# Performance work log

Hardware: AMD Instinct MI355X
Metric: run time of the kernel (lower is better)

## Reference

```python
import jax, jax.numpy as jnp
import numpy as np

WINDOWS = ((0, 4), (2, 6), (4, 8))
N_CLASSES = 64
EPS = 1e-12  # F.normalize eps


def setup_inputs() -> dict:
    key = jax.random.key(0)
    k1, k2 = jax.random.split(key)
    S, Q, T, D = 256, 4096, 8, 1024
    support_features = jax.random.normal(k1, (S, T, D), dtype=jnp.float32)
    target_features = jax.random.normal(k2, (Q, T, D), dtype=jnp.float32)
    support_labels = jnp.arange(S, dtype=jnp.int32) % N_CLASSES  # 4 shots per class, sorted-unique order
    logit_scale = jnp.array(0.0, dtype=jnp.float32)
    fusion_logits = jnp.zeros((3,), dtype=jnp.float32)
    return {
        'support_features': support_features,
        'target_features': target_features,
        'support_labels': support_labels,
        'logit_scale': logit_scale,
        'fusion_logits': fusion_logits,
    }


def _l2norm(x):
    n = jnp.sqrt(jnp.sum(x * x, axis=-1, keepdims=True))
    return x / jnp.maximum(n, EPS)


def _pairwise_dist(query_seq, support_seq):
    # query_seq: [Q, Tq, D], support_seq: [K, Ts, D] -> 1 - cosine sim [Q, K, Tq, Ts]
    sim = jnp.einsum('qtd,ksd->qkts', _l2norm(query_seq), _l2norm(support_seq))
    return 1.0 - sim


def _bi_mhm(dists):
    # dists: [Q, K, Tq, Ts]
    return dists.min(axis=3).sum(axis=2) + dists.min(axis=2).sum(axis=2)


def _segments(features):
    # features: [N, T, D] -> [N, n_windows, D] (mean over each window)
    return jnp.stack([features[:, s:e, :].mean(axis=1) for s, e in WINDOWS], axis=1)


def _prototypes(features, labels):
    # scatter-mean over class labels; features: [S, ...], labels: [S]
    sums = jax.ops.segment_sum(features, labels, num_segments=N_CLASSES)
    counts = jax.ops.segment_sum(jnp.ones((features.shape[0],), features.dtype), labels,
                                 num_segments=N_CLASSES)
    return sums / counts[:, None, None]


def reference(support_features, target_features, support_labels, logit_scale, fusion_logits):
    # global (frame-level) bidirectional min-sum chamfer distance to class prototypes
    support_proto = _prototypes(support_features, support_labels)          # [K, T, D]
    global_dist = _bi_mhm(_pairwise_dist(target_features, support_proto))  # [Q, K]

    # segment-level distances
    support_segments = _segments(support_features)                          # [S, 3, D]
    target_segments = _segments(target_features)                            # [Q, 3, D]
    support_seg_proto = _prototypes(support_segments, support_labels)       # [K, 3, D]
    seg_dist = _pairwise_dist(target_segments, support_seg_proto)           # [Q, K, 3, 3]
    seg_q2s = seg_dist.min(axis=3).sum(axis=2)
    seg_s2q = seg_dist.min(axis=2).sum(axis=2)

    fusion = jax.nn.softmax(fusion_logits)
    fused = (fusion[0] * global_dist + fusion[1] * seg_s2q + fusion[2] * seg_q2s)
    fused = fused * jnp.exp(logit_scale)
    return (-fused, -global_dist, -seg_s2q, -seg_q2s)
```

## Files before the change

### kernel.cpp

```cpp
#include <hip/hip_runtime.h>
#include <stdint.h>

typedef unsigned short u16;
typedef short short8 __attribute__((ext_vector_type(8)));
typedef float floatx4 __attribute__((ext_vector_type(4)));

#define KDIM 1024
#define QN   4096
#define KCLS 64
#define QK   (QN * KCLS)

#define DPP_XOR1 0xB1
#define DPP_XOR2 0x4E
#define DPP_HMIR 0x141
#define SWZ_XOR6  0x181F
#define SWZ_XOR16 0x401F

template <int CTRL>
__device__ __forceinline__ float dppf(float x) {
  int r = __builtin_amdgcn_mov_dpp(__builtin_bit_cast(int, x), CTRL, 0xF, 0xF, true);
  return __builtin_bit_cast(float, r);
}
template <int OFF>
__device__ __forceinline__ float swzf(float x) {
  int r = __builtin_amdgcn_ds_swizzle(__builtin_bit_cast(int, x), OFF);
  return __builtin_bit_cast(float, r);
}
__device__ __forceinline__ float max8(float x) {
  x = fmaxf(x, dppf<DPP_XOR1>(x));
  x = fmaxf(x, dppf<DPP_XOR2>(x));
  x = fmaxf(x, dppf<DPP_HMIR>(x));
  return x;
}
__device__ __forceinline__ float sum8(float x) {
  x += dppf<DPP_XOR1>(x);
  x += dppf<DPP_XOR2>(x);
  x += dppf<DPP_HMIR>(x);
  return x;
}


__device__ __forceinline__ u16 f2bf(float x) {
  union { float f; uint32_t u; } un; un.f = x;
  uint32_t u = un.u;
  u += 0x7FFFu + ((u >> 16) & 1u);
  return (u16)(u >> 16);
}

struct alignas(16) F4 { float x, y, z, w; };
struct alignas(8)  U16x4 { u16 a, b, c, d; };

__device__ __forceinline__ float dot4(const F4& a, const F4& b) {
  return a.x*b.x + a.y*b.y + a.z*b.z + a.w*b.w;
}

__device__ __forceinline__ void reduce11(float (&ss)[11], float (&tot)[11],
                                         float (*sb)[12], int lane, int wave) {
  #pragma unroll
  for (int v = 0; v < 11; ++v) {
    float x = ss[v];
    #pragma unroll
    for (int m = 1; m < 64; m <<= 1) x += __shfl_xor(x, m);
    ss[v] = x;
  }
  if (lane == 0) {
    #pragma unroll
    for (int v = 0; v < 11; ++v) sb[wave][v] = ss[v];
  }
  __syncthreads();
  #pragma unroll
  for (int v = 0; v < 11; ++v)
    tot[v] = sb[0][v] + sb[1][v] + sb[2][v] + sb[3][v];
}

__device__ __forceinline__ float inv_norm(float ss) {
  return 1.0f / fmaxf(sqrtf(ss), 1e-12f);
}

__global__ __launch_bounds__(256) void prep_all(const float* __restrict__ T,
                                                const float* __restrict__ S,
                                                u16* __restrict__ Ag,
                                                u16* __restrict__ Bg,
                                                float* __restrict__ invnT,
                                                float* __restrict__ invnTw,
                                                float* __restrict__ invnS,
                                                float* __restrict__ invnSw) {
  __shared__ float sb[4][12];
  const int b = blockIdx.x, tid = threadIdx.x;
  const int lane = tid & 63, wave = tid >> 6;

  if (b < QN) {
    const int q = b;
    F4 x[8];
    #pragma unroll
    for (int t = 0; t < 8; ++t)
      x[t] = *(const F4*)(T + (size_t)(q*8 + t)*1024 + tid*4);

    float ss[11], tot[11];
    #pragma unroll
    for (int t = 0; t < 8; ++t) ss[t] = dot4(x[t], x[t]);
    #pragma unroll
    for (int w = 0; w < 3; ++w) {
      F4 y;
      y.x = (x[2*w].x + x[2*w+1].x + x[2*w+2].x + x[2*w+3].x) * 0.25f;
      y.y = (x[2*w].y + x[2*w+1].y + x[2*w+2].y + x[2*w+3].y) * 0.25f;
      y.z = (x[2*w].z + x[2*w+1].z + x[2*w+2].z + x[2*w+3].z) * 0.25f;
      y.w = (x[2*w].w + x[2*w+1].w + x[2*w+2].w + x[2*w+3].w) * 0.25f;
      ss[8+w] = dot4(y, y);
    }
    reduce11(ss, tot, sb, lane, wave);

    #pragma unroll
    for (int t = 0; t < 8; ++t) {
      U16x4 o; o.a = f2bf(x[t].x); o.b = f2bf(x[t].y);
      o.c = f2bf(x[t].z); o.d = f2bf(x[t].w);
      *(U16x4*)(Ag + (size_t)(q*8 + t)*1024 + tid*4) = o;
    }
    if (tid < 8)       invnT [q*8 + tid]     = inv_norm(tot[tid]);
    else if (tid < 11) invnTw[q*4 + tid - 8] = inv_norm(tot[tid]);
  } else {
    const int k = b - QN;
    F4 p[8];
    #pragma unroll
    for (int t = 0; t < 8; ++t) { p[t].x = 0.f; p[t].y = 0.f; p[t].z = 0.f; p[t].w = 0.f; }
    #pragma unroll
    for (int s = 0; s < 4; ++s)
      #pragma unroll
      for (int t = 0; t < 8; ++t) {
        const F4 v = *(const F4*)(S + (size_t)(((s*64 + k)*8 + t))*1024 + tid*4);
        p[t].x += v.x; p[t].y += v.y; p[t].z += v.z; p[t].w += v.w;
      }
    float ss[11], tot[11];
    #pragma unroll
    for (int t = 0; t < 8; ++t) ss[t] = dot4(p[t], p[t]) * 0.0625f;
    #pragma unroll
    for (int w = 0; w < 3; ++w) {
      F4 y;
      y.x = (p[2*w].x + p[2*w+1].x + p[2*w+2].x + p[2*w+3].x) * 0.0625f;
      y.y = (p[2*w].y + p[2*w+1].y + p[2*w+2].y + p[2*w+3].y) * 0.0625f;
      y.z = (p[2*w].z + p[2*w+1].z + p[2*w+2].z + p[2*w+3].z) * 0.0625f;
      y.w = (p[2*w].w + p[2*w+1].w + p[2*w+2].w + p[2*w+3].w) * 0.0625f;
      ss[8+w] = dot4(y, y);
    }
    reduce11(ss, tot, sb, lane, wave);

    #pragma unroll
    for (int t = 0; t < 8; ++t) {
      U16x4 o; o.a = f2bf(p[t].x*0.25f); o.b = f2bf(p[t].y*0.25f);
      o.c = f2bf(p[t].z*0.25f); o.d = f2bf(p[t].w*0.25f);
      *(U16x4*)(Bg + (size_t)(k*8 + t)*1024 + tid*4) = o;
    }
    if (tid < 8)       invnS [k*8 + tid]     = inv_norm(tot[tid]);
    else if (tid < 11) invnSw[k*4 + tid - 8] = inv_norm(tot[tid]) * 0.0625f;
  }
}


__device__ __forceinline__ void load_lds16(const u16* g, u16* l) {
  __builtin_amdgcn_global_load_lds((__attribute__((address_space(1))) void*)(g),
                                   (__attribute__((address_space(3))) void*)(l),
                                   16, 0, 0);
}

__global__ __launch_bounds__(1024) void gemm_all(const u16* __restrict__ A,
                                                 const u16* __restrict__ B,
                                                 const float* __restrict__ invnT,
                                                 const float* __restrict__ invnTw,
                                                 const float* __restrict__ invnS,
                                                 const float* __restrict__ invnSw,
                                                 float* __restrict__ outF,
                                                 float* __restrict__ outG,
                                                 float* __restrict__ outS2Q,
                                                 float* __restrict__ outQ2S,
                                                 const float* __restrict__ fl,
                                                 const float* __restrict__ ls) {
  __shared__ __align__(16) u16 At[2][128 * 64];

  const int tid  = threadIdx.x;
  const int lane = tid & 63;
  const int wave = tid >> 6;
  const int wm = wave >> 3;
  const int wn = wave & 7;
  const int rowA0 = blockIdx.x * 128;

  floatx4 acc[4][4] = {};

  const int srow = lane >> 3;
  const int scol = ((lane & 7) ^ srow) * 8;
  const u16* aSrc = A + (size_t)(rowA0 + wave*8 + srow) * KDIM + scol;

  const u16* bBase = B + (size_t)(wn*64 + (lane & 15)) * KDIM + (lane >> 4) * 8;

  int aOff[4];
  #pragma unroll
  for (int i = 0; i < 4; ++i) {
    const int row = wm*64 + i*16 + (lane & 15);
    aOff[i] = row*64 + (((lane >> 4) ^ (row & 7)) * 8);
  }

  load_lds16(aSrc, &At[0][wave * 512]);

  for (int kb_i = 0; kb_i < 16; ++kb_i) {
    const int cur = kb_i & 1;
    __syncthreads();
    if (kb_i < 15)
      load_lds16(aSrc + (kb_i + 1) * 64, &At[cur ^ 1][wave * 512]);

    const u16* Ac = At[cur];
    #pragma unroll
    for (int kk = 0; kk < 2; ++kk) {
      short8 af[4], bf[4];
      #pragma unroll
      for (int i = 0; i < 4; ++i) {
        const int off = aOff[i] ^ (kk * 32);
        af[i] = *(const short8*)&Ac[off];
      }
      #pragma unroll
      for (int j = 0; j < 4; ++j)
        bf[j] = *(const short8*)(bBase + (size_t)j * 16 * KDIM + kb_i * 64 + kk * 32);
      #pragma unroll
      for (int i = 0; i < 4; ++i)
        #pragma unroll
        for (int j = 0; j < 4; ++j)
          acc[i][j] = __builtin_amdgcn_mfma_f32_16x16x32_bf16(af[i], bf[j], acc[i][j], 0, 0, 0);
    }
  }

  const int sIdx = lane & 7;
  const int b3 = (lane >> 3) & 1;
  const int b4 = (lane >> 4) & 1;
  const int b5 = lane >> 5;
  const int qL = blockIdx.x * 16 + wm * 8;
  const int kL = wn * 8;

  float invT[4][4], invTw3[4][3], invS[4], invSw3[4][3];
  #pragma unroll
  for (int i = 0; i < 4; ++i) {
    const int q = qL + i*2 + b5;
    #pragma unroll
    for (int r = 0; r < 4; ++r) invT[i][r] = invnT[q*8 + b4*4 + r];
    #pragma unroll
    for (int w = 0; w < 3; ++w) invTw3[i][w] = invnTw[q*4 + w];
  }
  #pragma unroll
  for (int j = 0; j < 4; ++j) {
    const int k = kL + j*2 + b3;
    invS[j] = invnS[k*8 + sIdx];
    #pragma unroll
    for (int v = 0; v < 3; ++v) invSw3[j][v] = invnSw[k*4 + v];
  }

  const float f0 = fl[0], f1 = fl[1], f2 = fl[2];
  const float mx = fmaxf(f0, fmaxf(f1, f2));
  const float e0 = __expf(f0 - mx), e1 = __expf(f1 - mx), e2 = __expf(f2 - mx);
  const float sc = __expf(ls[0]) / (e0 + e1 + e2);

  const int vA = (sIdx < 4) ? 0 : 2;
  const bool v1ok = (sIdx >= 2) && (sIdx <= 5);

  #pragma unroll
  for (int i = 0; i < 4; ++i) {
    #pragma unroll
    for (int j = 0; j < 4; ++j) {
      const floatx4 c = acc[i][j];

      float sim[4];
      #pragma unroll
      for (int r = 0; r < 4; ++r) sim[r] = c[r] * invT[i][r] * invS[j];
      float rs = 0.f;
      #pragma unroll
      for (int r = 0; r < 4; ++r) rs += max8(sim[r]);
      rs += swzf<SWZ_XOR16>(rs);
      float cm = fmaxf(fmaxf(sim[0], sim[1]), fmaxf(sim[2], sim[3]));
      cm = fmaxf(cm, swzf<SWZ_XOR16>(cm));
      const float cs = sum8(cm);
      const float g = rs + cs - 16.0f;

      float wA[4], wB[4];
      #pragma unroll
      for (int r = 0; r < 4; ++r) {
        const float p2 = c[r] + dppf<DPP_XOR1>(c[r]);
        wA[r] = p2 + dppf<DPP_XOR2>(p2);
        wB[r] = p2 + swzf<SWZ_XOR6>(p2);
      }
      float twA[3], twB[3];
      {
        const float aAll = wA[0] + wA[1] + wA[2] + wA[3];
        const float aOth = swzf<SWZ_XOR16>(aAll);
        twA[0] = b4 ? aOth : aAll;
        twA[2] = b4 ? aAll : aOth;
        const float aH = b4 ? (wA[0] + wA[1]) : (wA[2] + wA[3]);
        twA[1] = aH + swzf<SWZ_XOR16>(aH);
        const float bAll = wB[0] + wB[1] + wB[2] + wB[3];
        const float bOth = swzf<SWZ_XOR16>(bAll);
        twB[0] = b4 ? bOth : bAll;
        twB[2] = b4 ? bAll : bOth;
        const float bH = b4 ? (wB[0] + wB[1]) : (wB[2] + wB[3]);
        twB[1] = bH + swzf<SWZ_XOR16>(bH);
      }
      float pA[3], pB[3];
      #pragma unroll
      for (int w = 0; w < 3; ++w) {
        pA[w] = twA[w] * invTw3[i][w] * invSw3[j][vA];
        pB[w] = twB[w] * invTw3[i][w] * invSw3[j][1];
      }
      float q2s = 0.f;
      #pragma unroll
      for (int w = 0; w < 3; ++w)
        q2s += max8(v1ok ? fmaxf(pA[w], pB[w]) : pA[w]);
      const float mwA = fmaxf(fmaxf(pA[0], pA[1]), pA[2]);
      const float mwB = fmaxf(fmaxf(pB[0], pB[1]), pB[2]);
      float contrib = ((sIdx == 0) | (sIdx == 4)) ? mwA : 0.f;
      if (sIdx == 2) contrib += mwB;
      const float s2q = sum8(contrib);

      if ((lane & 23) == 0) {
        const int q = qL + i*2 + b5;
        const int k = kL + j*2 + b3;
        const size_t idx = (size_t)q * KCLS + k;
        const float o1 = g;
        const float o2 = s2q - 3.0f;
        const float o3 = q2s - 3.0f;
        outG[idx]   = o1;
        outS2Q[idx] = o2;
        outQ2S[idx] = o3;
        outF[idx]   = sc * (e0 * o1 + e1 * o2 + e2 * o3);
      }
    }
  }
}


extern "C" void kernel_launch(void* const* d_in, const int* in_sizes, int n_in,
                              void* d_out, int out_size, void* d_ws, size_t ws_size,
                              hipStream_t stream) {
  (void)in_sizes; (void)n_in; (void)out_size; (void)ws_size;
  const float* S  = (const float*)d_in[0];
  const float* T  = (const float*)d_in[1];
  const float* ls = (const float*)d_in[3];
  const float* fl = (const float*)d_in[4];

  float* outF   = (float*)d_out;
  float* outG   = outF + QK;
  float* outS2Q = outF + 2 * (size_t)QK;
  float* outQ2S = outF + 3 * (size_t)QK;

  u16*   Ag     = (u16*)d_ws;
  u16*   Bg     = Ag + (size_t)32768 * 1024;
  float* invnT  = (float*)(Bg + (size_t)512 * 1024);
  float* invnTw = invnT + 32768;
  float* invnS  = invnTw + 16384;
  float* invnSw = invnS + 512;

  prep_all<<<QN + KCLS, 256, 0, stream>>>(T, S, Ag, Bg, invnT, invnTw, invnS, invnSw);

  gemm_all<<<256, 1024, 0, stream>>>(Ag, Bg, invnT, invnTw, invnS, invnSw,
                                     outF, outG, outS2Q, outQ2S, fl, ls);
}
```

Before: 299.4 us.

## Retile GEMM to 128x128 blocks with A and B staged in LDS

Replaces the 1024-thread block, which covered 128 rows by all 512 B columns and read B fragments straight from global memory, with 256-thread blocks on a 2D grid, each computing a 128x128 tile. Both A and B tiles are loaded into swizzled LDS with direct global-to-LDS loads in 128-wide K chunks. The aim is to reuse B through LDS instead of repeated global reads and to raise the number of blocks for better occupancy. In exchange, A is now read four times, one per grid column, and the K loop loses double buffering, so each chunk's load is separated from compute by barriers.

```diff
diff --git a/kernel.cpp b/kernel.cpp
--- a/kernel.cpp
+++ b/kernel.cpp
@@ -162,62 +162,56 @@
                                    16, 0, 0);
 }
 
-__global__ __launch_bounds__(1024) void gemm_all(const u16* __restrict__ A,
-                                                 const u16* __restrict__ B,
-                                                 const float* __restrict__ invnT,
-                                                 const float* __restrict__ invnTw,
-                                                 const float* __restrict__ invnS,
-                                                 const float* __restrict__ invnSw,
-                                                 float* __restrict__ outF,
-                                                 float* __restrict__ outG,
-                                                 float* __restrict__ outS2Q,
-                                                 float* __restrict__ outQ2S,
-                                                 const float* __restrict__ fl,
-                                                 const float* __restrict__ ls) {
-  __shared__ __align__(16) u16 At[2][128 * 64];
+__global__ __launch_bounds__(256) void gemm_all(const u16* __restrict__ A,
+                                                const u16* __restrict__ B,
+                                                const float* __restrict__ invnT,
+                                                const float* __restrict__ invnTw,
+                                                const float* __restrict__ invnS,
+                                                const float* __restrict__ invnSw,
+                                                float* __restrict__ outF,
+                                                float* __restrict__ outG,
+                                                float* __restrict__ outS2Q,
+                                                float* __restrict__ outQ2S,
+                                                const float* __restrict__ fl,
+                                                const float* __restrict__ ls) {
+  __shared__ __align__(16) u16 At[128 * 128];
+  __shared__ __align__(16) u16 Bt[128 * 128];
 
   const int tid  = threadIdx.x;
   const int lane = tid & 63;
   const int wave = tid >> 6;
-  const int wm = wave >> 3;
-  const int wn = wave & 7;
+  const int wm = wave >> 1, wn = wave & 1;
   const int rowA0 = blockIdx.x * 128;
+  const int rowB0 = blockIdx.y * 128;
 
   floatx4 acc[4][4] = {};
 
-  const int srow = lane >> 3;
-  const int scol = ((lane & 7) ^ srow) * 8;
-  const u16* aSrc = A + (size_t)(rowA0 + wave*8 + srow) * KDIM + scol;
-
-  const u16* bBase = B + (size_t)(wn*64 + (lane & 15)) * KDIM + (lane >> 4) * 8;
-
-  int aOff[4];
-  #pragma unroll
-  for (int i = 0; i < 4; ++i) {
-    const int row = wm*64 + i*16 + (lane & 15);
-    aOff[i] = row*64 + (((lane >> 4) ^ (row & 7)) * 8);
-  }
-
-  load_lds16(aSrc, &At[0][wave * 512]);
-
-  for (int kb_i = 0; kb_i < 16; ++kb_i) {
-    const int cur = kb_i & 1;
+  const int srow = lane >> 4;
+  const int sl   = lane & 15;
+
+  for (int kb = 0; kb < KDIM; kb += 128) {
     __syncthreads();
-    if (kb_i < 15)
-      load_lds16(aSrc + (kb_i + 1) * 64, &At[cur ^ 1][wave * 512]);
-
-    const u16* Ac = At[cur];
-    #pragma unroll
-    for (int kk = 0; kk < 2; ++kk) {
+    #pragma unroll
+    for (int it = 0; it < 8; ++it) {
+      const int c   = wave * 8 + it;
+      const int row = c * 4 + srow;
+      const int scol = ((sl ^ (row & 7)) * 8);
+      load_lds16(A + (size_t)(rowA0 + row) * KDIM + kb + scol, &At[c * 512]);
+      load_lds16(B + (size_t)(rowB0 + row) * KDIM + kb + scol, &Bt[c * 512]);
+    }
+    __syncthreads();
+    const int q4 = lane >> 4;
+    #pragma unroll
+    for (int kk = 0; kk < 4; ++kk) {
+      const int kc0 = kk * 4 + q4;
       short8 af[4], bf[4];
       #pragma unroll
       for (int i = 0; i < 4; ++i) {
-        const int off = aOff[i] ^ (kk * 32);
-        af[i] = *(const short8*)&Ac[off];
-      }
-      #pragma unroll
-      for (int j = 0; j < 4; ++j)
-        bf[j] = *(const short8*)(bBase + (size_t)j * 16 * KDIM + kb_i * 64 + kk * 32);
+        const int row = wm*64 + i*16 + (lane & 15);
+        af[i] = *(const short8*)&At[row*128 + ((kc0 ^ (row & 7)) * 8)];
+        const int col = wn*64 + i*16 + (lane & 15);
+        bf[i] = *(const short8*)&Bt[col*128 + ((kc0 ^ (col & 7)) * 8)];
+      }
       #pragma unroll
       for (int i = 0; i < 4; ++i)
         #pragma unroll
@@ -231,7 +225,7 @@
   const int b4 = (lane >> 4) & 1;
   const int b5 = lane >> 5;
   const int qL = blockIdx.x * 16 + wm * 8;
-  const int kL = wn * 8;
+  const int kL = blockIdx.y * 16 + wn * 8;
 
   float invT[4][4], invTw3[4][3], invS[4], invSw3[4][3];
   #pragma unroll
@@ -354,6 +348,6 @@
 
   prep_all<<<QN + KCLS, 256, 0, stream>>>(T, S, Ag, Bg, invnT, invnTw, invnS, invnSw);
 
-  gemm_all<<<256, 1024, 0, stream>>>(Ag, Bg, invnT, invnTw, invnS, invnSw,
-                                     outF, outG, outS2Q, outQ2S, fl, ls);
-}
+  gemm_all<<<dim3(256, 4), 256, 0, stream>>>(Ag, Bg, invnT, invnTw, invnS, invnSw,
+                                             outF, outG, outS2Q, outQ2S, fl, ls);
+}
```

Result: faster. 269.3 us (-10.0%).
